# Optimization experiments

Hardware: AMD Instinct MI355X
Metric: run time of the kernel (lower is better)

Reference implementation:

```python
import jax, jax.numpy as jnp
import numpy as np

N, IN_DIM, D, H, L, E, MAX_DEG = 50000, 128, 128, 16, 3, 800000, 512
C = D // H  # head dim


def _ln(x, scale, bias, eps=1e-5):
    mu = x.mean(-1, keepdims=True)
    var = ((x - mu) ** 2).mean(-1, keepdims=True)
    return (x - mu) * jax.lax.rsqrt(var + eps) * scale + bias


def setup_inputs() -> dict:
    key = jax.random.key(0)
    ks = jax.random.split(key, 20)
    s = 0.02
    inp = {
        "x": jax.random.normal(ks[0], (N, IN_DIM), jnp.float32),
        "edge_index": jax.random.randint(ks[1], (2, E), 0, N, jnp.int32),
        "W_in": jax.random.normal(ks[2], (IN_DIM, D), jnp.float32) * s,
        "b_in": jnp.zeros((D,), jnp.float32),
        "in_emb": jax.random.normal(ks[3], (MAX_DEG + 1, D), jnp.float32) * s,
        "out_emb": jax.random.normal(ks[4], (MAX_DEG + 1, D), jnp.float32) * s,
        "ln_scale": jnp.ones((L, D), jnp.float32),
        "ln_bias": jnp.zeros((L, D), jnp.float32),
        "Wq": jax.random.normal(ks[5], (L, D, D), jnp.float32) * s,
        "bq": jnp.zeros((L, D), jnp.float32),
        "Wk": jax.random.normal(ks[6], (L, D, D), jnp.float32) * s,
        "bk": jnp.zeros((L, D), jnp.float32),
        "Wv": jax.random.normal(ks[7], (L, D, D), jnp.float32) * s,
        "bv": jnp.zeros((L, D), jnp.float32),
        "Wskip": jax.random.normal(ks[8], (L, D, D), jnp.float32) * s,
        "bskip": jnp.zeros((L, D), jnp.float32),
        "Wbeta": jax.random.normal(ks[9], (L, 3 * D, 1), jnp.float32) * s,
        "fn_scale": jnp.ones((D,), jnp.float32),
        "fn_bias": jnp.zeros((D,), jnp.float32),
    }
    return inp


def _transformer_conv(h, src, tgt, Wq, bq, Wk, bk, Wv, bv, Wskip, bskip, Wbeta):
    # PyG TransformerConv, beta=True, concat=True, eval mode (no dropout)
    q = (h @ Wq + bq).reshape(N, H, C)
    k = (h @ Wk + bk).reshape(N, H, C)
    v = (h @ Wv + bv).reshape(N, H, C)
    # per-edge attention logits [E, H]
    alpha = (q[tgt] * k[src]).sum(-1) / jnp.sqrt(jnp.float32(C))
    # scatter-softmax over incoming edges of each target node
    m = jax.ops.segment_max(alpha, tgt, num_segments=N)
    ex = jnp.exp(alpha - m[tgt])
    den = jax.ops.segment_sum(ex, tgt, num_segments=N)
    w = ex / den[tgt]  # [E, H]
    msg = v[src] * w[:, :, None]  # [E, H, C]
    out = jax.ops.segment_sum(msg, tgt, num_segments=N).reshape(N, D)
    # root skip + gated beta combination
    xr = h @ Wskip + bskip
    beta = jax.nn.sigmoid(jnp.concatenate([out, xr, out - xr], axis=-1) @ Wbeta)
    return beta * xr + (1.0 - beta) * out


def reference(x, edge_index, W_in, b_in, in_emb, out_emb, ln_scale, ln_bias,
              Wq, bq, Wk, bk, Wv, bv, Wskip, bskip, Wbeta, fn_scale, fn_bias):
    src, tgt = edge_index[0], edge_index[1]
    h = x @ W_in + b_in
    # centrality encoding: in/out degree embeddings
    ones = jnp.ones((E,), jnp.float32)
    idg = jnp.clip(jax.ops.segment_sum(ones, tgt, num_segments=N), 0, MAX_DEG).astype(jnp.int32)
    odg = jnp.clip(jax.ops.segment_sum(ones, src, num_segments=N), 0, MAX_DEG).astype(jnp.int32)
    h = h + in_emb[idg] + out_emb[odg]
    for l in range(L):
        hn = _ln(h, ln_scale[l], ln_bias[l])
        h = h + _transformer_conv(hn, src, tgt, Wq[l], bq[l], Wk[l], bk[l],
                                  Wv[l], bv[l], Wskip[l], bskip[l], Wbeta[l])
    return _ln(h, fn_scale, fn_bias)
```

## Files before the change

kernel.cpp:

```cpp
#include <hip/hip_runtime.h>
#include <math.h>
#include <stdint.h>

#define NN 50000
#define DM 128
#define NH 16
#define HC 8
#define NL 3
#define NE 800000
#define MAXDEG 512
#define NRG 1563

#define NB2 782
#define NBLK 256
#define CNTN (NB2 * NBLK)
#define SC1 196
#define RNG 4
#define REP 16

typedef __attribute__((ext_vector_type(8))) short short8;
typedef __attribute__((ext_vector_type(4))) float f32x4;
typedef __attribute__((ext_vector_type(2))) float f32x2;

static __device__ __forceinline__ unsigned short f2bf(float x) {
    union { float f; unsigned int u; } v; v.f = x;
    unsigned int r = (v.u + 0x7fffu + ((v.u >> 16) & 1u)) >> 16;
    return (unsigned short)r;
}
static __device__ __forceinline__ float bf2f(unsigned short b) {
    union { unsigned int u; float f; } v; v.u = ((unsigned int)b) << 16;
    return v.f;
}

__global__ __launch_bounds__(1024) void hist_out_kernel(const int* __restrict__ ei,
                                                        unsigned int* __restrict__ part) {
    __shared__ unsigned int hp[8192];
    int rg = blockIdx.x;
    int rp = blockIdx.y;
    int t = threadIdx.x;
    for (int i = t; i < 8192; i += 1024) hp[i] = 0;
    __syncthreads();
    int lo = rg << 14;
    for (int e = rp * 1024 + t; e < NE; e += REP * 1024) {
        int s = ei[e] - lo;
        if ((unsigned)s < 16384u)
            atomicAdd(&hp[s >> 1], (s & 1) ? 0x10000u : 1u);
    }
    __syncthreads();
    unsigned int* pp = part + (size_t)(rg * REP + rp) * 8192;
    for (int i = t; i < 8192; i += 1024) pp[i] = hp[i];
}
__global__ __launch_bounds__(256) void hist_reduce_kernel(const unsigned int* __restrict__ part,
                                                          int* __restrict__ outdeg) {
    int wd = blockIdx.x * 256 + threadIdx.x;
    if (wd >= 25000) return;
    int rg = wd >> 13, lw = wd & 8191;
    unsigned int sum = 0;
#pragma unroll
    for (int r = 0; r < REP; r++)
        sum += part[(size_t)(rg * REP + r) * 8192 + lw];
    outdeg[2 * wd] = sum & 0xffff;
    if (2 * wd + 1 < NN) outdeg[2 * wd + 1] = sum >> 16;
}

__global__ __launch_bounds__(256) void p1_count_kernel(const int* __restrict__ ei,
                                                       int* __restrict__ cnt) {
    __shared__ int hh[NB2];
    int t = threadIdx.x, blk = blockIdx.x;
    for (int b = t; b < NB2; b += 256) hh[b] = 0;
    __syncthreads();
    for (int e = blk * 256 + t; e < NE; e += NBLK * 256)
        atomicAdd(&hh[ei[NE + e] >> 6], 1);
    __syncthreads();
    for (int b = t; b < NB2; b += 256) cnt[b * NBLK + blk] = hh[b];
}

__global__ __launch_bounds__(1024) void gscan1_kernel(int* __restrict__ data,
                                                      int* __restrict__ bsum, int n) {
    __shared__ int sd[1024];
    int t = threadIdx.x;
    int i = blockIdx.x * 1024 + t;
    int val = (i < n) ? data[i] : 0;
    sd[t] = val;
    __syncthreads();
    for (int d = 1; d < 1024; d <<= 1) {
        int x = (t >= d) ? sd[t - d] : 0;
        __syncthreads();
        sd[t] += x;
        __syncthreads();
    }
    if (i < n) data[i] = sd[t] - val;
    if (t == 1023) bsum[blockIdx.x] = sd[1023];
}
__global__ void gscan2_kernel(const int* __restrict__ bsum, int* __restrict__ bpre, int nb) {
    int run = 0;
    for (int i = 0; i < nb; i++) { bpre[i] = run; run += bsum[i]; }
}
__global__ __launch_bounds__(1024) void gscan3_kernel(int* __restrict__ data,
                                                      const int* __restrict__ bpre, int n) {
    int i = blockIdx.x * 1024 + threadIdx.x;
    if (i < n) data[i] += bpre[blockIdx.x];
}

__global__ __launch_bounds__(256) void p3_scatter_kernel(const int* __restrict__ ei,
                                                         const int* __restrict__ cnt,
                                                         int* __restrict__ tmp) {
    __shared__ int hh[NB2];
    int t = threadIdx.x, blk = blockIdx.x;
    for (int b = t; b < NB2; b += 256) hh[b] = cnt[b * NBLK + blk];
    __syncthreads();
    for (int e = blk * 256 + t; e < NE; e += NBLK * 256) {
        int s = ei[e], tg = ei[NE + e];
        int pos = atomicAdd(&hh[tg >> 6], 1);
        tmp[pos] = ((tg & 63) << 16) | s;
    }
}

__global__ __launch_bounds__(256) void p4_fine_kernel(const int* __restrict__ tmp,
                                                      const int* __restrict__ cnt,
                                                      int* __restrict__ off,
                                                      int* __restrict__ indeg,
                                                      int* __restrict__ srcs) {
    __shared__ int c64[64], x64[64], cur[64];
    int b = blockIdx.x, t = threadIdx.x;
    int e0 = cnt[b * NBLK];
    int e1 = (b == NB2 - 1) ? NE : cnt[(b + 1) * NBLK];
    if (t < 64) c64[t] = 0;
    __syncthreads();
    for (int i = e0 + t; i < e1; i += 256) atomicAdd(&c64[(tmp[i] >> 16) & 63], 1);
    __syncthreads();
    if (t == 0) {
        int run = 0;
        for (int j = 0; j < 64; j++) { x64[j] = run; cur[j] = e0 + run; run += c64[j]; }
    }
    __syncthreads();
    if (t < 64) {
        int node = b * 64 + t;
        if (node <= NN) off[node] = e0 + x64[t];
        if (node < NN) indeg[node] = c64[t];
    }
    __syncthreads();
    for (int i = e0 + t; i < e1; i += 256) {
        int w = tmp[i];
        int pos = atomicAdd(&cur[(w >> 16) & 63], 1);
        srcs[pos] = w & 0xffff;
    }
}

__global__ __launch_bounds__(256) void wprep_kernel(const float* __restrict__ Wq,
                                                    const float* __restrict__ Wk,
                                                    const float* __restrict__ Wv,
                                                    const float* __restrict__ Ws,
                                                    const float* __restrict__ Win,
                                                    unsigned short* __restrict__ Wt) {
    __shared__ unsigned short lds[128 * 130];
    int bid = blockIdx.x;
    const float* W;
    if (bid == 12) {
        W = Win;
    } else {
        int l = bid >> 2, m = bid & 3;
        W = (m == 0 ? Wq : m == 1 ? Wk : m == 2 ? Wv : Ws) + (size_t)l * DM * DM;
    }
    unsigned short* out = Wt + (size_t)bid * DM * DM;
    int t = threadIdx.x;
    for (int i = t; i < DM * DM; i += 256) {
        int kk = i >> 7, c = i & 127;
        lds[kk * 130 + c] = f2bf(W[i]);
    }
    __syncthreads();
    for (int o = t; o < DM * DM; o += 256) {
        int c = o >> 7, kk = o & 127;
        out[o] = lds[kk * 130 + c];
    }
}

__global__ __launch_bounds__(256) void xcast_kernel(const float* __restrict__ x,
                                                    unsigned short* __restrict__ xb) {
    int i = blockIdx.x * 256 + threadIdx.x;
    float4 xv = ((const float4*)x)[i];
    ushort4 o;
    o.x = f2bf(xv.x); o.y = f2bf(xv.y); o.z = f2bf(xv.z); o.w = f2bf(xv.w);
    ((ushort4*)xb)[i] = o;
}

__global__ __launch_bounds__(256) void gemm_in_mfma(const unsigned short* __restrict__ xb,
                                                    const unsigned short* __restrict__ Wt,
                                                    const float* __restrict__ b,
                                                    const float* __restrict__ in_emb,
                                                    const float* __restrict__ out_emb,
                                                    const int* __restrict__ indeg,
                                                    const int* __restrict__ outdeg,
                                                    float* __restrict__ h) {
    int w = threadIdx.x >> 6;
    int l = threadIdx.x & 63;
    int lr = l & 15, lc = l >> 4;
    int colbase = (w & 1) * 64;
    int rhalf = w >> 1;

    short8 bfrag[4][4];
#pragma unroll
    for (int ct = 0; ct < 4; ct++) {
        const unsigned short* bp = Wt + (size_t)(colbase + ct * 16 + lr) * DM;
#pragma unroll
        for (int kk = 0; kk < 4; kk++)
            bfrag[ct][kk] = *(const short8*)(bp + kk * 32 + lc * 8);
    }

    for (int rg = blockIdx.x * 2 + rhalf; rg < NRG; rg += gridDim.x * 2) {
        int n0 = rg * 32;
        short8 afrag[2][4];
#pragma unroll
        for (int rt = 0; rt < 2; rt++) {
            int row = n0 + rt * 16 + lr;
            if (row >= NN) row = NN - 1;
            const unsigned short* ap = xb + (size_t)row * DM;
#pragma unroll
            for (int kk = 0; kk < 4; kk++)
                afrag[rt][kk] = *(const short8*)(ap + kk * 32 + lc * 8);
        }
        f32x4 acc[4][2];
#pragma unroll
        for (int ct = 0; ct < 4; ct++)
#pragma unroll
            for (int nt = 0; nt < 2; nt++)
                acc[ct][nt] = (f32x4){0.f, 0.f, 0.f, 0.f};
#pragma unroll
        for (int kk = 0; kk < 4; kk++)
#pragma unroll
            for (int ct = 0; ct < 4; ct++)
#pragma unroll
                for (int nt = 0; nt < 2; nt++)
                    acc[ct][nt] = __builtin_amdgcn_mfma_f32_16x16x32_bf16(
                        bfrag[ct][kk], afrag[nt][kk], acc[ct][nt], 0, 0, 0);
#pragma unroll
        for (int nt = 0; nt < 2; nt++) {
            int node = n0 + nt * 16 + lr;
            if (node < NN) {
                int id = min(indeg[node], MAXDEG);
                int od = min(outdeg[node], MAXDEG);
#pragma unroll
                for (int ct = 0; ct < 4; ct++) {
                    int ch = colbase + ct * 16 + lc * 4;
                    float4 bb = *(const float4*)(b + ch);
                    float4 ie = *(const float4*)(in_emb + (size_t)id * DM + ch);
                    float4 oe = *(const float4*)(out_emb + (size_t)od * DM + ch);
                    float4 o;
                    o.x = acc[ct][nt][0] + bb.x + ie.x + oe.x;
                    o.y = acc[ct][nt][1] + bb.y + ie.y + oe.y;
                    o.z = acc[ct][nt][2] + bb.z + ie.z + oe.z;
                    o.w = acc[ct][nt][3] + bb.w + ie.w + oe.w;
                    *(float4*)(h + (size_t)node * DM + ch) = o;
                }
            }
        }
    }
}

static __device__ __forceinline__ void ln_body(const float* __restrict__ hp,
                                               const float* __restrict__ sc,
                                               const float* __restrict__ bi,
                                               int lane, float* o0, float* o1) {
    float v0 = hp[lane], v1 = hp[lane + 64];
    float s = v0 + v1;
#pragma unroll
    for (int d = 32; d; d >>= 1) s += __shfl_xor(s, d);
    float mu = s * (1.f / 128.f);
    float d0 = v0 - mu, d1 = v1 - mu;
    float vs = d0 * d0 + d1 * d1;
#pragma unroll
    for (int d = 32; d; d >>= 1) vs += __shfl_xor(vs, d);
    float rstd = rsqrtf(vs * (1.f / 128.f) + 1e-5f);
    *o0 = d0 * rstd * sc[lane] + bi[lane];
    *o1 = d1 * rstd * sc[lane + 64] + bi[lane + 64];
}

__global__ __launch_bounds__(256) void ln_bf16_kernel(const float* __restrict__ h,
                                                      const float* __restrict__ sc,
                                                      const float* __restrict__ bi,
                                                      unsigned short* __restrict__ o) {
    int row = blockIdx.x * 4 + (threadIdx.x >> 6);
    int lane = threadIdx.x & 63;
    float a, b;
    ln_body(h + (size_t)row * DM, sc, bi, lane, &a, &b);
    unsigned short* op = o + (size_t)row * DM;
    op[lane] = f2bf(a);
    op[lane + 64] = f2bf(b);
}

__global__ __launch_bounds__(512) void gemm_qkvs_mfma(const unsigned short* __restrict__ hn,
                                                      const unsigned short* __restrict__ Wt,
                                                      const float* __restrict__ bq, const float* __restrict__ bk,
                                                      const float* __restrict__ bv, const float* __restrict__ bs,
                                                      unsigned short* __restrict__ q,
                                                      unsigned char* __restrict__ kv8,
                                                      unsigned short* __restrict__ xrb) {
    int w = threadIdx.x >> 6;
    int l = threadIdx.x & 63;
    int lr = l & 15, lc = l >> 4;
    int colbase = w * 64;
    int m = w >> 1;
    int cmbase = (w & 1) * 64;

    const float* bptr = (m == 0 ? bq : m == 1 ? bk : m == 2 ? bv : bs);
    short8 bfrag[4][4];
    float biasv[4][4];
#pragma unroll
    for (int ct = 0; ct < 4; ct++) {
        int col = colbase + ct * 16 + lr;
        const unsigned short* bp = Wt + (size_t)col * DM;
#pragma unroll
        for (int kk = 0; kk < 4; kk++)
            bfrag[ct][kk] = *(const short8*)(bp + kk * 32 + lc * 8);
#pragma unroll
        for (int j = 0; j < 4; j++)
            biasv[ct][j] = bptr[cmbase + ct * 16 + lc * 4 + j];
    }

    for (int rg = blockIdx.x; rg < NRG; rg += gridDim.x) {
        int n0 = rg * 32;
        short8 afrag[2][4];
#pragma unroll
        for (int nt = 0; nt < 2; nt++) {
            int row = n0 + nt * 16 + lr;
            if (row >= NN) row = NN - 1;
            const unsigned short* ap = hn + (size_t)row * DM;
#pragma unroll
            for (int kk = 0; kk < 4; kk++)
                afrag[nt][kk] = *(const short8*)(ap + kk * 32 + lc * 8);
        }
        f32x4 acc[4][2];
#pragma unroll
        for (int ct = 0; ct < 4; ct++)
#pragma unroll
            for (int nt = 0; nt < 2; nt++)
                acc[ct][nt] = (f32x4){0.f, 0.f, 0.f, 0.f};
#pragma unroll
        for (int kk = 0; kk < 4; kk++)
#pragma unroll
            for (int ct = 0; ct < 4; ct++)
#pragma unroll
                for (int nt = 0; nt < 2; nt++)
                    acc[ct][nt] = __builtin_amdgcn_mfma_f32_16x16x32_bf16(
                        bfrag[ct][kk], afrag[nt][kk], acc[ct][nt], 0, 0, 0);

        if (m == 0 || m == 3) {
            unsigned short* dst = (m == 0) ? q : xrb;
#pragma unroll
            for (int nt = 0; nt < 2; nt++) {
                int node = n0 + nt * 16 + lr;
                if (node < NN) {
#pragma unroll
                    for (int ct = 0; ct < 4; ct++) {
                        int ch = cmbase + ct * 16 + lc * 4;
                        ushort4 st;
                        st.x = f2bf(acc[ct][nt][0] + biasv[ct][0]);
                        st.y = f2bf(acc[ct][nt][1] + biasv[ct][1]);
                        st.z = f2bf(acc[ct][nt][2] + biasv[ct][2]);
                        st.w = f2bf(acc[ct][nt][3] + biasv[ct][3]);
                        *(ushort4*)(dst + (size_t)node * DM + ch) = st;
                    }
                }
            }
        } else {
            unsigned char* base = kv8 + ((m == 1) ? 0 : 4);
#pragma unroll
            for (int nt = 0; nt < 2; nt++) {
                int node = n0 + nt * 16 + lr;
                if (node < NN) {
#pragma unroll
                    for (int ct = 0; ct < 4; ct++) {
                        int ch = cmbase + ct * 16 + lc * 4;
                        int wd = __builtin_amdgcn_cvt_pk_fp8_f32(
                            acc[ct][nt][0] + biasv[ct][0],
                            acc[ct][nt][1] + biasv[ct][1], 0, false);
                        wd = __builtin_amdgcn_cvt_pk_fp8_f32(
                            acc[ct][nt][2] + biasv[ct][2],
                            acc[ct][nt][3] + biasv[ct][3], wd, true);
                        *(unsigned int*)(base + (size_t)node * 256 + (ch >> 2) * 8) =
                            (unsigned int)wd;
                    }
                }
            }
        }
    }
}

__global__ __launch_bounds__(256) void attn_fused_kernel(const int* __restrict__ off,
                                                         const int* __restrict__ srcs,
                                                         const unsigned short* __restrict__ q,
                                                         const unsigned char* __restrict__ kv8,
                                                         const unsigned short* __restrict__ xrb,
                                                         const float* __restrict__ Wb,
                                                         float* __restrict__ h,
                                                         const float* __restrict__ nsc,
                                                         const float* __restrict__ nbi,
                                                         unsigned short* __restrict__ hn_out,
                                                         const float* __restrict__ fsc,
                                                         const float* __restrict__ fbi,
                                                         float* __restrict__ fout) {
    int wv = threadIdx.x >> 6;
    int L = threadIdx.x & 63;
    int half = L >> 5, L5 = L & 31;
    int n = blockIdx.x * 4 + wv;
    int o0 = off[n], o1 = off[n + 1];
    int c4 = L5 * 4;
    const float isq = 0.35355339059f;

    ushort4 qu = *(const ushort4*)(q + (size_t)n * DM + c4);
    float q0 = bf2f(qu.x) * isq, q1 = bf2f(qu.y) * isq,
          q2 = bf2f(qu.z) * isq, q3 = bf2f(qu.w) * isq;

    float den = 0.f, a0 = 0.f, a1 = 0.f, a2 = 0.f, a3 = 0.f;
    int p = o0;
    for (; p + 16 <= o1; p += 16) {
        int sj[8];
#pragma unroll
        for (int j = 0; j < 8; j++) sj[j] = srcs[p + 2 * j + half];
        uint2 uu[8];
#pragma unroll
        for (int j = 0; j < 8; j++)
            uu[j] = *(const uint2*)(kv8 + (size_t)sj[j] * 256 + L5 * 8);
#pragma unroll
        for (int j = 0; j < 8; j++) {
            f32x2 k01 = __builtin_amdgcn_cvt_pk_f32_fp8(uu[j].x, false);
            f32x2 k23 = __builtin_amdgcn_cvt_pk_f32_fp8(uu[j].x, true);
            f32x2 v01 = __builtin_amdgcn_cvt_pk_f32_fp8(uu[j].y, false);
            f32x2 v23 = __builtin_amdgcn_cvt_pk_f32_fp8(uu[j].y, true);
            float d = q0 * k01.x + q1 * k01.y + q2 * k23.x + q3 * k23.y;
            d += __shfl_xor(d, 1);
            float e2 = __expf(d);
            den += e2;
            a0 += e2 * v01.x;
            a1 += e2 * v01.y;
            a2 += e2 * v23.x;
            a3 += e2 * v23.y;
        }
    }
    if (p < o1) {
        int sj[8];
#pragma unroll
        for (int j = 0; j < 8; j++) {
            int e = p + 2 * j + half;
            sj[j] = (e < o1) ? srcs[e] : 0;
        }
        uint2 uu[8];
#pragma unroll
        for (int j = 0; j < 8; j++)
            uu[j] = *(const uint2*)(kv8 + (size_t)sj[j] * 256 + L5 * 8);
#pragma unroll
        for (int j = 0; j < 8; j++) {
            int e = p + 2 * j + half;
            f32x2 k01 = __builtin_amdgcn_cvt_pk_f32_fp8(uu[j].x, false);
            f32x2 k23 = __builtin_amdgcn_cvt_pk_f32_fp8(uu[j].x, true);
            f32x2 v01 = __builtin_amdgcn_cvt_pk_f32_fp8(uu[j].y, false);
            f32x2 v23 = __builtin_amdgcn_cvt_pk_f32_fp8(uu[j].y, true);
            float d = q0 * k01.x + q1 * k01.y + q2 * k23.x + q3 * k23.y;
            d += __shfl_xor(d, 1);
            float e2 = (e < o1) ? __expf(d) : 0.f;
            den += e2;
            a0 += e2 * v01.x;
            a1 += e2 * v01.y;
            a2 += e2 * v23.x;
            a3 += e2 * v23.y;
        }
    }
    den += __shfl_xor(den, 32);
    a0 += __shfl_xor(a0, 32);
    a1 += __shfl_xor(a1, 32);
    a2 += __shfl_xor(a2, 32);
    a3 += __shfl_xor(a3, 32);

    float inv = (den > 0.f) ? 1.f / den : 0.f;
    float o0v = a0 * inv, o1v = a1 * inv, o2v = a2 * inv, o3v = a3 * inv;

    ushort4 xu = *(const ushort4*)(xrb + (size_t)n * DM + c4);
    float x0 = bf2f(xu.x), x1 = bf2f(xu.y), x2 = bf2f(xu.z), x3 = bf2f(xu.w);
    float c = o0v * Wb[c4] + o1v * Wb[c4 + 1] + o2v * Wb[c4 + 2] + o3v * Wb[c4 + 3]
            + x0 * Wb[DM + c4] + x1 * Wb[DM + c4 + 1]
            + x2 * Wb[DM + c4 + 2] + x3 * Wb[DM + c4 + 3]
            + (o0v - x0) * Wb[2 * DM + c4] + (o1v - x1) * Wb[2 * DM + c4 + 1]
            + (o2v - x2) * Wb[2 * DM + c4 + 2] + (o3v - x3) * Wb[2 * DM + c4 + 3];
    if (half) c = 0.f;
#pragma unroll
    for (int d2 = 32; d2; d2 >>= 1) c += __shfl_xor(c, d2);
    float beta = 1.f / (1.f + __expf(-c));

    size_t idx = (size_t)n * DM + c4;
    float4 hv = *(const float4*)(h + idx);
    hv.x += beta * x0 + (1.f - beta) * o0v;
    hv.y += beta * x1 + (1.f - beta) * o1v;
    hv.z += beta * x2 + (1.f - beta) * o2v;
    hv.w += beta * x3 + (1.f - beta) * o3v;

    if (fout) {
        float s = hv.x + hv.y + hv.z + hv.w;
#pragma unroll
        for (int d2 = 16; d2; d2 >>= 1) s += __shfl_xor(s, d2);
        float mu = s * (1.f / 128.f);
        float d0 = hv.x - mu, d1 = hv.y - mu, d2_ = hv.z - mu, d3 = hv.w - mu;
        float vs = d0 * d0 + d1 * d1 + d2_ * d2_ + d3 * d3;
#pragma unroll
        for (int d2 = 16; d2; d2 >>= 1) vs += __shfl_xor(vs, d2);
        float rstd = rsqrtf(vs * (1.f / 128.f) + 1e-5f);
        if (half == 0) {
            float4 scv = *(const float4*)(fsc + c4);
            float4 biv = *(const float4*)(fbi + c4);
            float4 o;
            o.x = d0 * rstd * scv.x + biv.x;
            o.y = d1 * rstd * scv.y + biv.y;
            o.z = d2_ * rstd * scv.z + biv.z;
            o.w = d3 * rstd * scv.w + biv.w;
            *(float4*)(fout + idx) = o;
        }
    } else {
        if (half == 0) *(float4*)(h + idx) = hv;
        float s = hv.x + hv.y + hv.z + hv.w;
#pragma unroll
        for (int d2 = 16; d2; d2 >>= 1) s += __shfl_xor(s, d2);
        float mu = s * (1.f / 128.f);
        float d0 = hv.x - mu, d1 = hv.y - mu, d2_ = hv.z - mu, d3 = hv.w - mu;
        float vs = d0 * d0 + d1 * d1 + d2_ * d2_ + d3 * d3;
#pragma unroll
        for (int d2 = 16; d2; d2 >>= 1) vs += __shfl_xor(vs, d2);
        float rstd = rsqrtf(vs * (1.f / 128.f) + 1e-5f);
        if (half == 0) {
            float4 scv = *(const float4*)(nsc + c4);
            float4 biv = *(const float4*)(nbi + c4);
            ushort4 o;
            o.x = f2bf(d0 * rstd * scv.x + biv.x);
            o.y = f2bf(d1 * rstd * scv.y + biv.y);
            o.z = f2bf(d2_ * rstd * scv.z + biv.z);
            o.w = f2bf(d3 * rstd * scv.w + biv.w);
            *(ushort4*)(hn_out + idx) = o;
        }
    }
}

static inline char* alignup(char* p) {
    return (char*)(((uintptr_t)p + 255) & ~(uintptr_t)255);
}

extern "C" void kernel_launch(void* const* d_in, const int* in_sizes, int n_in,
                              void* d_out, int out_size, void* d_ws, size_t ws_size,
                              hipStream_t stream) {
    const float* x       = (const float*)d_in[0];
    const int*   ei      = (const int*)d_in[1];
    const float* W_in    = (const float*)d_in[2];
    const float* b_in    = (const float*)d_in[3];
    const float* in_emb  = (const float*)d_in[4];
    const float* out_emb = (const float*)d_in[5];
    const float* ln_sc   = (const float*)d_in[6];
    const float* ln_bi   = (const float*)d_in[7];
    const float* Wq      = (const float*)d_in[8];
    const float* bq      = (const float*)d_in[9];
    const float* Wk      = (const float*)d_in[10];
    const float* bk      = (const float*)d_in[11];
    const float* Wv      = (const float*)d_in[12];
    const float* bv      = (const float*)d_in[13];
    const float* Wsk     = (const float*)d_in[14];
    const float* bsk     = (const float*)d_in[15];
    const float* Wbeta   = (const float*)d_in[16];
    const float* fn_sc   = (const float*)d_in[17];
    const float* fn_bi   = (const float*)d_in[18];

    char* w = (char*)d_ws;
    int* indeg  = (int*)w; w = alignup(w + (size_t)NN * 4);
    int* outdeg = (int*)w; w = alignup(w + (size_t)NN * 4);
    int* off    = (int*)w; w = alignup(w + (size_t)(NN + 1) * 4);
    int* srcs   = (int*)w; w = alignup(w + (size_t)NE * 4);
    int* tmp    = (int*)w; w = alignup(w + (size_t)NE * 4);
    int* cnt    = (int*)w; w = alignup(w + (size_t)CNTN * 4);
    int* bsum   = (int*)w; w = alignup(w + (size_t)SC1 * 4);
    int* bpre   = (int*)w; w = alignup(w + (size_t)SC1 * 4);
    unsigned int* hpart = (unsigned int*)w; w = alignup(w + (size_t)RNG * REP * 8192 * 4);
    float* h    = (float*)w; w = alignup(w + (size_t)NN * DM * 4);
    unsigned short* hn  = (unsigned short*)w; w = alignup(w + (size_t)NN * DM * 2);
    unsigned short* q   = (unsigned short*)w; w = alignup(w + (size_t)NN * DM * 2);
    unsigned short* xrb = (unsigned short*)w; w = alignup(w + (size_t)NN * DM * 2);
    unsigned char*  kv8 = (unsigned char*)w;  w = alignup(w + (size_t)NN * 256);
    unsigned short* xb  = (unsigned short*)w; w = alignup(w + (size_t)NN * DM * 2);
    unsigned short* Wt  = (unsigned short*)w; w = alignup(w + (size_t)13 * DM * DM * 2);

    hist_out_kernel<<<dim3(RNG, REP), 1024, 0, stream>>>(ei, hpart);
    hist_reduce_kernel<<<98, 256, 0, stream>>>(hpart, outdeg);
    p1_count_kernel<<<NBLK, 256, 0, stream>>>(ei, cnt);
    gscan1_kernel<<<SC1, 1024, 0, stream>>>(cnt, bsum, CNTN);
    gscan2_kernel<<<1, 1, 0, stream>>>(bsum, bpre, SC1);
    gscan3_kernel<<<SC1, 1024, 0, stream>>>(cnt, bpre, CNTN);
    p3_scatter_kernel<<<NBLK, 256, 0, stream>>>(ei, cnt, tmp);
    p4_fine_kernel<<<NB2, 256, 0, stream>>>(tmp, cnt, off, indeg, srcs);

    wprep_kernel<<<13, 256, 0, stream>>>(Wq, Wk, Wv, Wsk, W_in, Wt);
    xcast_kernel<<<NN * DM / 4 / 256, 256, 0, stream>>>(x, xb);

    gemm_in_mfma<<<391, 256, 0, stream>>>(xb, Wt + (size_t)12 * DM * DM, b_in,
                                          in_emb, out_emb, indeg, outdeg, h);
    ln_bf16_kernel<<<NN / 4, 256, 0, stream>>>(h, ln_sc, ln_bi, hn);
    for (int l = 0; l < NL; l++) {
        gemm_qkvs_mfma<<<391, 512, 0, stream>>>(hn,
            Wt + (size_t)l * 4 * DM * DM,
            bq + l * DM, bk + l * DM, bv + l * DM, bsk + l * DM,
            q, kv8, xrb);
        bool last = (l == NL - 1);
        attn_fused_kernel<<<NN / 4, 256, 0, stream>>>(off, srcs, q, kv8, xrb,
            Wbeta + (size_t)l * 3 * DM, h,
            last ? (const float*)nullptr : ln_sc + (l + 1) * DM,
            last ? (const float*)nullptr : ln_bi + (l + 1) * DM,
            last ? (unsigned short*)nullptr : hn,
            last ? fn_sc : (const float*)nullptr,
            last ? fn_bi : (const float*)nullptr,
            last ? (float*)d_out : (float*)nullptr);
    }
}
```

Measured before the change: 353.4 us.

## Fuse first LayerNorm into input GEMM and stage QKVS A-tiles through swizzled LDS

Folds the initial LayerNorm into the input-projection GEMM epilogue. Row sums and sums of squares are reduced across lanes, and the two wave halves of a row exchange partials through shared memory, so the separate ln_bf16 kernel and its re-read of h go away. The QKVS GEMM now loads each 32-row A tile once per block with coalesced 16-byte loads into an XOR-swizzled LDS buffer, instead of each of the 8 waves re-reading the same rows from global memory. It adds block-wide barriers, and the fused LayerNorm switches to the E[x^2]-mu^2 variance form, which is slightly less numerically robust.

```diff
diff --git a/kernel.cpp b/kernel.cpp
--- a/kernel.cpp
+++ b/kernel.cpp
@@ -191,7 +191,11 @@
                                                     const float* __restrict__ out_emb,
                                                     const int* __restrict__ indeg,
                                                     const int* __restrict__ outdeg,
-                                                    float* __restrict__ h) {
+                                                    float* __restrict__ h,
+                                                    const float* __restrict__ nsc,
+                                                    const float* __restrict__ nbi,
+                                                    unsigned short* __restrict__ hn) {
+    __shared__ f32x2 pp[4][2][16];
     int w = threadIdx.x >> 6;
     int l = threadIdx.x & 63;
     int lr = l & 15, lc = l >> 4;
@@ -207,38 +211,46 @@
             bfrag[ct][kk] = *(const short8*)(bp + kk * 32 + lc * 8);
     }
 
-    for (int rg = blockIdx.x * 2 + rhalf; rg < NRG; rg += gridDim.x * 2) {
+    for (int it = blockIdx.x; it < 782; it += gridDim.x) {
+        int rg = it * 2 + rhalf;
+        bool act = (rg < NRG);
         int n0 = rg * 32;
-        short8 afrag[2][4];
-#pragma unroll
-        for (int rt = 0; rt < 2; rt++) {
-            int row = n0 + rt * 16 + lr;
-            if (row >= NN) row = NN - 1;
-            const unsigned short* ap = xb + (size_t)row * DM;
+        float hval[2][16];
+        float s2[2], q2[2];
+        s2[0] = s2[1] = q2[0] = q2[1] = 0.f;
+
+        if (act) {
+            short8 afrag[2][4];
+#pragma unroll
+            for (int nt = 0; nt < 2; nt++) {
+                int row = n0 + nt * 16 + lr;
+                if (row >= NN) row = NN - 1;
+                const unsigned short* ap = xb + (size_t)row * DM;
+#pragma unroll
+                for (int kk = 0; kk < 4; kk++)
+                    afrag[nt][kk] = *(const short8*)(ap + kk * 32 + lc * 8);
+            }
+            f32x4 acc[4][2];
+#pragma unroll
+            for (int ct = 0; ct < 4; ct++)
+#pragma unroll
+                for (int nt = 0; nt < 2; nt++)
+                    acc[ct][nt] = (f32x4){0.f, 0.f, 0.f, 0.f};
 #pragma unroll
             for (int kk = 0; kk < 4; kk++)
-                afrag[rt][kk] = *(const short8*)(ap + kk * 32 + lc * 8);
-        }
-        f32x4 acc[4][2];
-#pragma unroll
-        for (int ct = 0; ct < 4; ct++)
-#pragma unroll
-            for (int nt = 0; nt < 2; nt++)
-                acc[ct][nt] = (f32x4){0.f, 0.f, 0.f, 0.f};
-#pragma unroll
-        for (int kk = 0; kk < 4; kk++)
-#pragma unroll
-            for (int ct = 0; ct < 4; ct++)
-#pragma unroll
-                for (int nt = 0; nt < 2; nt++)
-                    acc[ct][nt] = __builtin_amdgcn_mfma_f32_16x16x32_bf16(
-                        bfrag[ct][kk], afrag[nt][kk], acc[ct][nt], 0, 0, 0);
-#pragma unroll
-        for (int nt = 0; nt < 2; nt++) {
-            int node = n0 + nt * 16 + lr;
-            if (node < NN) {
-                int id = min(indeg[node], MAXDEG);
-                int od = min(outdeg[node], MAXDEG);
+#pragma unroll
+                for (int ct = 0; ct < 4; ct++)
+#pragma unroll
+                    for (int nt = 0; nt < 2; nt++)
+                        acc[ct][nt] = __builtin_amdgcn_mfma_f32_16x16x32_bf16(
+                            bfrag[ct][kk], afrag[nt][kk], acc[ct][nt], 0, 0, 0);
+#pragma unroll
+            for (int nt = 0; nt < 2; nt++) {
+                int node = n0 + nt * 16 + lr;
+                int nodec = (node < NN) ? node : (NN - 1);
+                int id = min(indeg[nodec], MAXDEG);
+                int od = min(outdeg[nodec], MAXDEG);
+                float s = 0.f, sq = 0.f;
 #pragma unroll
                 for (int ct = 0; ct < 4; ct++) {
                     int ch = colbase + ct * 16 + lc * 4;
@@ -250,42 +262,53 @@
                     o.y = acc[ct][nt][1] + bb.y + ie.y + oe.y;
                     o.z = acc[ct][nt][2] + bb.z + ie.z + oe.z;
                     o.w = acc[ct][nt][3] + bb.w + ie.w + oe.w;
-                    *(float4*)(h + (size_t)node * DM + ch) = o;
+                    hval[nt][ct * 4 + 0] = o.x;
+                    hval[nt][ct * 4 + 1] = o.y;
+                    hval[nt][ct * 4 + 2] = o.z;
+                    hval[nt][ct * 4 + 3] = o.w;
+                    s += o.x + o.y + o.z + o.w;
+                    sq += o.x * o.x + o.y * o.y + o.z * o.z + o.w * o.w;
+                    if (node < NN)
+                        *(float4*)(h + (size_t)node * DM + ch) = o;
+                }
+                s += __shfl_xor(s, 16); s += __shfl_xor(s, 32);
+                sq += __shfl_xor(sq, 16); sq += __shfl_xor(sq, 32);
+                s2[nt] = s; q2[nt] = sq;
+            }
+        }
+        __syncthreads();
+        if (act && lc == 0) {
+            pp[w][0][lr] = (f32x2){s2[0], q2[0]};
+            pp[w][1][lr] = (f32x2){s2[1], q2[1]};
+        }
+        __syncthreads();
+        if (act) {
+#pragma unroll
+            for (int nt = 0; nt < 2; nt++) {
+                f32x2 po = pp[w ^ 1][nt][lr];
+                float S = s2[nt] + po.x;
+                float Q = q2[nt] + po.y;
+                float mu = S * (1.f / 128.f);
+                float var = Q * (1.f / 128.f) - mu * mu;
+                float rstd = rsqrtf(var + 1e-5f);
+                int node = n0 + nt * 16 + lr;
+                if (node < NN) {
+#pragma unroll
+                    for (int ct = 0; ct < 4; ct++) {
+                        int ch = colbase + ct * 16 + lc * 4;
+                        float4 scv = *(const float4*)(nsc + ch);
+                        float4 biv = *(const float4*)(nbi + ch);
+                        ushort4 o;
+                        o.x = f2bf((hval[nt][ct * 4 + 0] - mu) * rstd * scv.x + biv.x);
+                        o.y = f2bf((hval[nt][ct * 4 + 1] - mu) * rstd * scv.y + biv.y);
+                        o.z = f2bf((hval[nt][ct * 4 + 2] - mu) * rstd * scv.z + biv.z);
+                        o.w = f2bf((hval[nt][ct * 4 + 3] - mu) * rstd * scv.w + biv.w);
+                        *(ushort4*)(hn + (size_t)node * DM + ch) = o;
+                    }
                 }
             }
         }
     }
-}
-
-static __device__ __forceinline__ void ln_body(const float* __restrict__ hp,
-                                               const float* __restrict__ sc,
-                                               const float* __restrict__ bi,
-                                               int lane, float* o0, float* o1) {
-    float v0 = hp[lane], v1 = hp[lane + 64];
-    float s = v0 + v1;
-#pragma unroll
-    for (int d = 32; d; d >>= 1) s += __shfl_xor(s, d);
-    float mu = s * (1.f / 128.f);
-    float d0 = v0 - mu, d1 = v1 - mu;
-    float vs = d0 * d0 + d1 * d1;
-#pragma unroll
-    for (int d = 32; d; d >>= 1) vs += __shfl_xor(vs, d);
-    float rstd = rsqrtf(vs * (1.f / 128.f) + 1e-5f);
-    *o0 = d0 * rstd * sc[lane] + bi[lane];
-    *o1 = d1 * rstd * sc[lane + 64] + bi[lane + 64];
-}
-
-__global__ __launch_bounds__(256) void ln_bf16_kernel(const float* __restrict__ h,
-                                                      const float* __restrict__ sc,
-                                                      const float* __restrict__ bi,
-                                                      unsigned short* __restrict__ o) {
-    int row = blockIdx.x * 4 + (threadIdx.x >> 6);
-    int lane = threadIdx.x & 63;
-    float a, b;
-    ln_body(h + (size_t)row * DM, sc, bi, lane, &a, &b);
-    unsigned short* op = o + (size_t)row * DM;
-    op[lane] = f2bf(a);
-    op[lane + 64] = f2bf(b);
 }
 
 __global__ __launch_bounds__(512) void gemm_qkvs_mfma(const unsigned short* __restrict__ hn,
@@ -295,12 +318,19 @@
                                                       unsigned short* __restrict__ q,
                                                       unsigned char* __restrict__ kv8,
                                                       unsigned short* __restrict__ xrb) {
+    __shared__ uint4 alds4[512];
+    unsigned short* alds = (unsigned short*)alds4;
+
     int w = threadIdx.x >> 6;
     int l = threadIdx.x & 63;
     int lr = l & 15, lc = l >> 4;
     int colbase = w * 64;
     int m = w >> 1;
     int cmbase = (w & 1) * 64;
+    int t = threadIdx.x;
+    int ar = t >> 4;
+    int ag = t & 15;
+    int agx = ag ^ (ar & 7);
 
     const float* bptr = (m == 0 ? bq : m == 1 ? bk : m == 2 ? bv : bs);
     short8 bfrag[4][4];
@@ -319,16 +349,23 @@
 
     for (int rg = blockIdx.x; rg < NRG; rg += gridDim.x) {
         int n0 = rg * 32;
+        int grow = n0 + ar;
+        if (grow >= NN) grow = NN - 1;
+        uint4 av = *(const uint4*)(hn + (size_t)grow * DM + ag * 8);
+        __syncthreads();
+        alds4[ar * 16 + agx] = av;
+        __syncthreads();
+
         short8 afrag[2][4];
 #pragma unroll
-        for (int nt = 0; nt < 2; nt++) {
-            int row = n0 + nt * 16 + lr;
-            if (row >= NN) row = NN - 1;
-            const unsigned short* ap = hn + (size_t)row * DM;
-#pragma unroll
-            for (int kk = 0; kk < 4; kk++)
-                afrag[nt][kk] = *(const short8*)(ap + kk * 32 + lc * 8);
-        }
+        for (int nt = 0; nt < 2; nt++)
+#pragma unroll
+            for (int kk = 0; kk < 4; kk++) {
+                int g = kk * 4 + lc;
+                int gx = g ^ (lr & 7);
+                afrag[nt][kk] = *(const short8*)(alds + (nt * 16 + lr) * 128 + gx * 8);
+            }
+
         f32x4 acc[4][2];
 #pragma unroll
         for (int ct = 0; ct < 4; ct++)
@@ -595,8 +632,8 @@
     xcast_kernel<<<NN * DM / 4 / 256, 256, 0, stream>>>(x, xb);
 
     gemm_in_mfma<<<391, 256, 0, stream>>>(xb, Wt + (size_t)12 * DM * DM, b_in,
-                                          in_emb, out_emb, indeg, outdeg, h);
-    ln_bf16_kernel<<<NN / 4, 256, 0, stream>>>(h, ln_sc, ln_bi, hn);
+                                          in_emb, out_emb, indeg, outdeg, h,
+                                          ln_sc, ln_bi, hn);
     for (int l = 0; l < NL; l++) {
         gemm_qkvs_mfma<<<391, 512, 0, stream>>>(hn,
             Wt + (size_t)l * 4 * DM * DM,
```

After: 332.4 us (median of 2 runs). 1.06x faster.
